# Performance work log

Measured on AMD Instinct MI355X. Metric: run time of the kernel, lower is better.

Reference implementation:

```python
import jax, jax.numpy as jnp
import numpy as np

T, DIM, HID = 8192, 1024, 4096

def setup_inputs() -> dict:
    key = jax.random.key(0)
    k1, k2, k3 = jax.random.split(key, 3)
    x = jax.random.normal(k1, (T, DIM), dtype=jnp.float32)
    # torch Linear weight layout: [out_features, in_features]
    W_fc = jax.random.normal(k2, (HID, DIM), dtype=jnp.float32) * 0.02
    W_proj = jax.random.normal(k3, (DIM, HID), dtype=jnp.float32) * 0.02
    return {"x": x, "W_fc": W_fc, "W_proj": W_proj}

def reference(x, W_fc, W_proj):
    # fc: x @ W_fc^T  -> relu -> square -> proj: @ W_proj^T
    h = jnp.einsum('td,hd->th', x, W_fc)      # [T, HID]
    h = jnp.square(jax.nn.relu(h))            # relu(h)^2 (relu^2 activation)
    return jnp.einsum('th,dh->td', h, W_proj) # [T, DIM]
```

## Files before the change

### kernel.cpp

```cpp
#include <hip/hip_runtime.h>
#include <stdint.h>


#define BM 128
#define BN 128
#define BK 64

typedef __attribute__((ext_vector_type(8))) short bf16x8;
typedef __attribute__((ext_vector_type(4))) float f32x4;

typedef const __attribute__((address_space(1))) unsigned int* gas_u32p;
typedef __attribute__((address_space(3))) unsigned int* las_u32p;

__device__ __forceinline__ void load16_to_lds(const void* gptr, void* lptr) {
    __builtin_amdgcn_global_load_lds((gas_u32p)gptr, (las_u32p)lptr, 16, 0, 0);
}

__device__ __forceinline__ unsigned short f2bf(float f) {
    unsigned int u = __float_as_uint(f);
    u += 0x7FFFu + ((u >> 16) & 1u);
    return (unsigned short)(u >> 16);
}

__global__ void cvt_all(const float4* __restrict__ x,  ushort4* __restrict__ xb,
                        const float4* __restrict__ wf, ushort4* __restrict__ wfb,
                        const float4* __restrict__ wp, ushort4* __restrict__ wpb)
{
    const int base = blockIdx.x * 1024 + threadIdx.x;
    #pragma unroll
    for (int j = 0; j < 4; j++) {
        const int i = base + j * 256;
        const float4* s; ushort4* d; int k;
        if (i < (1 << 21))            { s = x;  d = xb;  k = i; }
        else if (i < 3 * (1 << 20))   { s = wf; d = wfb; k = i - (1 << 21); }
        else                          { s = wp; d = wpb; k = i - 3 * (1 << 20); }
        float4 v = s[k];
        ushort4 o;
        o.x = f2bf(v.x); o.y = f2bf(v.y); o.z = f2bf(v.z); o.w = f2bf(v.w);
        d[k] = o;
    }
}

template<bool RELU2, bool OUT_BF16>
__global__ __launch_bounds__(256, 3)
void gemm_bt(const unsigned short* __restrict__ A,
             const unsigned short* __restrict__ B,
             void* __restrict__ Cv, int M, int N, int K)
{
    __shared__ unsigned short sA[BM * BK];
    __shared__ unsigned short sB[BN * BK];

    const int tid  = threadIdx.x;
    const int lane = tid & 63;
    const int wave = tid >> 6;
    const int wm   = (wave >> 1) * 64;
    const int wn   = (wave & 1) * 64;
    const int quad = lane >> 4;
    const int m16  = lane & 15;

    const long bm0 = (long)blockIdx.y * BM;
    const long bn0 = (long)blockIdx.x * BN;

    const int srow = tid >> 3;
    const int scol = (tid & 7) * 8;

    const unsigned short* gA = A + (bm0 + srow) * (long)K + scol;
    const unsigned short* gB = B + (bn0 + srow) * (long)K + scol;
    char* lA = (char*)sA + tid * 16;
    char* lB = (char*)sB + tid * 16;

    f32x4 acc[4][4];
    #pragma unroll
    for (int i = 0; i < 4; i++)
        #pragma unroll
        for (int j = 0; j < 4; j++)
            acc[i][j] = (f32x4)0.0f;

    for (int k0 = 0; k0 < K; k0 += BK) {
        #pragma unroll
        for (int c = 0; c < 4; c++)
            load16_to_lds(gA + (long)c * 32 * K + k0, lA + c * 4096);
        #pragma unroll
        for (int c = 0; c < 4; c++)
            load16_to_lds(gB + (long)c * 32 * K + k0, lB + c * 4096);
        __syncthreads();

        #pragma unroll
        for (int h = 0; h < 2; h++) {
            bf16x8 af[4], bfr[4];
            #pragma unroll
            for (int i = 0; i < 4; i++)
                af[i]  = *(const bf16x8*)&sA[(wm + i * 16 + m16) * BK + h * 32 + quad * 8];
            #pragma unroll
            for (int j = 0; j < 4; j++)
                bfr[j] = *(const bf16x8*)&sB[(wn + j * 16 + m16) * BK + h * 32 + quad * 8];

            #pragma unroll
            for (int i = 0; i < 4; i++)
                #pragma unroll
                for (int j = 0; j < 4; j++)
                    acc[i][j] = __builtin_amdgcn_mfma_f32_16x16x32_bf16(
                        af[i], bfr[j], acc[i][j], 0, 0, 0);
        }
        __syncthreads();
    }

    #pragma unroll
    for (int i = 0; i < 4; i++) {
        #pragma unroll
        for (int j = 0; j < 4; j++) {
            #pragma unroll
            for (int r = 0; r < 4; r++) {
                float v = acc[i][j][r];
                if (RELU2) v = (v > 0.0f) ? v * v : 0.0f;
                const long row = bm0 + wm + i * 16 + quad * 4 + r;
                const long col = bn0 + wn + j * 16 + m16;
                if (OUT_BF16)
                    ((unsigned short*)Cv)[row * (long)N + col] = f2bf(v);
                else
                    ((float*)Cv)[row * (long)N + col] = v;
            }
        }
    }
}

extern "C" void kernel_launch(void* const* d_in, const int* in_sizes, int n_in,
                              void* d_out, int out_size, void* d_ws, size_t ws_size,
                              hipStream_t stream) {
    (void)in_sizes; (void)n_in; (void)out_size; (void)ws_size;

    const int T = 8192, DIM = 1024, HID = 4096;

    const float* x     = (const float*)d_in[0];
    const float* W_fc  = (const float*)d_in[1];
    const float* W_prj = (const float*)d_in[2];
    float* out = (float*)d_out;

    char* ws = (char*)d_ws;
    unsigned short* h   = (unsigned short*)ws;
    unsigned short* xb  = (unsigned short*)(ws + (64l << 20));
    unsigned short* wfb = (unsigned short*)(ws + (80l << 20));
    unsigned short* wpb = (unsigned short*)(ws + (88l << 20));

    cvt_all<<<4096, 256, 0, stream>>>(
        (const float4*)x,     (ushort4*)xb,
        (const float4*)W_fc,  (ushort4*)wfb,
        (const float4*)W_prj, (ushort4*)wpb);

    gemm_bt<true, true><<<dim3(HID / BN, T / BM), dim3(256), 0, stream>>>(
        xb, wfb, h, T, HID, DIM);

    gemm_bt<false, false><<<dim3(DIM / BN, T / BM), dim3(256), 0, stream>>>(
        h, wpb, out, T, DIM, HID);
}
```

Measured before the change: 273.9 us.

## Replace GEMM with 8-wave 256-row tiled, double-buffered pipelined kernel

Replaces the 128x128 single-buffer GEMM with a 512-thread kernel that uses 256-row tiles and NF-dependent column tiles. It double-buffers LDS so the next k-slices are prefetched while MFMAs run, using interleaved barriers, explicit vmcnt waits and setprio. It also XOR-swizzles LDS offsets to avoid bank conflicts and remaps block IDs across 8 groups for cache locality. The cost is heavier register and LDS use per block, plus fragile hand-tuned wait counts.

```diff
diff --git a/kernel.cpp b/kernel.cpp
--- a/kernel.cpp
+++ b/kernel.cpp
@@ -1,10 +1,6 @@
 #include <hip/hip_runtime.h>
 #include <stdint.h>
 
-
-#define BM 128
-#define BN 128
-#define BK 64
 
 typedef __attribute__((ext_vector_type(8))) short bf16x8;
 typedef __attribute__((ext_vector_type(4))) float f32x4;
@@ -41,80 +37,179 @@
     }
 }
 
-template<bool RELU2, bool OUT_BF16>
-__global__ __launch_bounds__(256, 3)
-void gemm_bt(const unsigned short* __restrict__ A,
-             const unsigned short* __restrict__ B,
-             void* __restrict__ Cv, int M, int N, int K)
+#define LGKM0_FENCE() do { \
+    asm volatile("s_waitcnt lgkmcnt(0)" ::: "memory"); \
+    __builtin_amdgcn_sched_barrier(0); } while (0)
+
+template<int NF, bool RELU2, bool OUT_BF16>
+__global__ __launch_bounds__(512, 2)
+void gemm8p(const unsigned short* __restrict__ A,
+            const unsigned short* __restrict__ B,
+            void* __restrict__ Cv, int M, int N, int K)
 {
-    __shared__ unsigned short sA[BM * BK];
-    __shared__ unsigned short sB[BN * BK];
+    constexpr int BM   = 256;
+    constexpr int BN   = 64 * NF;
+    constexpr int CB   = BN / 128;
+    constexpr int AKH  = 16384;
+    constexpr int BKH  = BN * 64;
+    constexpr int BOFF = 2 * AKH;
+    constexpr int BUFB = 2 * AKH + 2 * BKH;
+    constexpr int KEEP = 2 + 2 * CB;
+    (void)M;
+
+    __shared__ char lds[2 * BUFB];
 
     const int tid  = threadIdx.x;
     const int lane = tid & 63;
     const int wave = tid >> 6;
-    const int wm   = (wave >> 1) * 64;
-    const int wn   = (wave & 1) * 64;
+    const int wm   = wave >> 2;
+    const int wn   = wave & 3;
     const int quad = lane >> 4;
     const int m16  = lane & 15;
 
-    const long bm0 = (long)blockIdx.y * BM;
-    const long bn0 = (long)blockIdx.x * BN;
-
-    const int srow = tid >> 3;
-    const int scol = (tid & 7) * 8;
-
-    const unsigned short* gA = A + (bm0 + srow) * (long)K + scol;
-    const unsigned short* gB = B + (bn0 + srow) * (long)K + scol;
-    char* lA = (char*)sA + tid * 16;
-    char* lB = (char*)sB + tid * 16;
-
-    f32x4 acc[4][4];
-    #pragma unroll
-    for (int i = 0; i < 4; i++)
-        #pragma unroll
-        for (int j = 0; j < 4; j++)
+    const int gx = gridDim.x;
+    int flat = blockIdx.y * gx + blockIdx.x;
+    const int cpx = (gx * gridDim.y) >> 3;
+    flat = (flat & 7) * cpx + (flat >> 3);
+    const long bm0 = (long)(flat / gx) * BM;
+    const long bn0 = (long)(flat % gx) * BN;
+
+    const int srow   = tid >> 2;
+    const int schunk = (tid & 3) ^ ((tid >> 3) & 3);
+    const unsigned short* gA = A + (bm0 + srow) * (long)K + schunk * 8;
+    const unsigned short* gB = B + (bn0 + srow) * (long)K + schunk * 8;
+    char* lbase = (char*)lds;
+
+    int offA[8], offB[NF];
+    #pragma unroll
+    for (int i = 0; i < 8; i++) {
+        const int lo = (wm * 128 + i * 16 + m16) * 64 + quad * 16;
+        offA[i] = lo ^ (((lo >> 7) & 3) << 4);
+    }
+    #pragma unroll
+    for (int j = 0; j < NF; j++) {
+        const int lo = (wn * 16 * NF + j * 16 + m16) * 64 + quad * 16;
+        offB[j] = lo ^ (((lo >> 7) & 3) << 4);
+    }
+
+    f32x4 acc[8][NF];
+    #pragma unroll
+    for (int i = 0; i < 8; i++)
+        #pragma unroll
+        for (int j = 0; j < NF; j++)
             acc[i][j] = (f32x4)0.0f;
 
-    for (int k0 = 0; k0 < K; k0 += BK) {
-        #pragma unroll
-        for (int c = 0; c < 4; c++)
-            load16_to_lds(gA + (long)c * 32 * K + k0, lA + c * 4096);
-        #pragma unroll
-        for (int c = 0; c < 4; c++)
-            load16_to_lds(gB + (long)c * 32 * K + k0, lB + c * 4096);
-        __syncthreads();
-
-        #pragma unroll
-        for (int h = 0; h < 2; h++) {
-            bf16x8 af[4], bfr[4];
-            #pragma unroll
-            for (int i = 0; i < 4; i++)
-                af[i]  = *(const bf16x8*)&sA[(wm + i * 16 + m16) * BK + h * 32 + quad * 8];
-            #pragma unroll
-            for (int j = 0; j < 4; j++)
-                bfr[j] = *(const bf16x8*)&sB[(wn + j * 16 + m16) * BK + h * 32 + quad * 8];
-
-            #pragma unroll
-            for (int i = 0; i < 4; i++)
-                #pragma unroll
-                for (int j = 0; j < 4; j++)
-                    acc[i][j] = __builtin_amdgcn_mfma_f32_16x16x32_bf16(
-                        af[i], bfr[j], acc[i][j], 0, 0, 0);
-        }
-        __syncthreads();
-    }
-
-    #pragma unroll
-    for (int i = 0; i < 4; i++) {
-        #pragma unroll
-        for (int j = 0; j < 4; j++) {
+    const int NT = K >> 6;
+
+    #define STAGE_A(t, kh) do { \
+        char* _d = lbase + ((t) & 1) * BUFB + (kh) * AKH + tid * 16; \
+        const unsigned short* _s = gA + (long)(t) * 64 + (kh) * 32; \
+        load16_to_lds(_s, _d); \
+        load16_to_lds(_s + 128l * K, _d + 8192); } while (0)
+
+    #define STAGE_B(t, kh) do { \
+        char* _d = lbase + ((t) & 1) * BUFB + BOFF + (kh) * BKH + tid * 16; \
+        const unsigned short* _s = gB + (long)(t) * 64 + (kh) * 32; \
+        load16_to_lds(_s, _d); \
+        if (CB == 2) load16_to_lds(_s + 128l * K, _d + 8192); } while (0)
+
+    STAGE_B(0, 0); STAGE_A(0, 0); STAGE_B(0, 1); STAGE_A(0, 1);
+    if (NT > 1) {
+        STAGE_B(1, 0); STAGE_A(1, 0); STAGE_B(1, 1);
+        asm volatile("s_waitcnt vmcnt(%0)" :: "i"(KEEP) : "memory");
+    } else {
+        asm volatile("s_waitcnt vmcnt(0)" ::: "memory");
+    }
+    __builtin_amdgcn_sched_barrier(0);
+    __builtin_amdgcn_s_barrier();
+
+    for (int t = 0; t < NT; ++t) {
+        char* bufA = lbase + (t & 1) * BUFB;
+        char* bufB = bufA + BOFF;
+        bf16x8 af[4], bf[NF];
+
+        #pragma unroll
+        for (int j = 0; j < NF; j++) bf[j] = *(const bf16x8*)(bufB + offB[j]);
+        #pragma unroll
+        for (int i = 0; i < 4; i++)  af[i] = *(const bf16x8*)(bufA + offA[i]);
+        if (t + 1 < NT) STAGE_A(t + 1, 1);
+        __builtin_amdgcn_s_barrier();
+        LGKM0_FENCE();
+        __builtin_amdgcn_s_setprio(1);
+        #pragma unroll
+        for (int i = 0; i < 4; i++)
+            #pragma unroll
+            for (int j = 0; j < NF; j++)
+                acc[i][j] = __builtin_amdgcn_mfma_f32_16x16x32_bf16(
+                    af[i], bf[j], acc[i][j], 0, 0, 0);
+        __builtin_amdgcn_s_setprio(0);
+        __builtin_amdgcn_s_barrier();
+
+        #pragma unroll
+        for (int i = 0; i < 4; i++)  af[i] = *(const bf16x8*)(bufA + offA[4 + i]);
+        if (t + 2 < NT) STAGE_B(t + 2, 0);
+        __builtin_amdgcn_s_barrier();
+        LGKM0_FENCE();
+        __builtin_amdgcn_s_setprio(1);
+        #pragma unroll
+        for (int i = 0; i < 4; i++)
+            #pragma unroll
+            for (int j = 0; j < NF; j++)
+                acc[4 + i][j] = __builtin_amdgcn_mfma_f32_16x16x32_bf16(
+                    af[i], bf[j], acc[4 + i][j], 0, 0, 0);
+        __builtin_amdgcn_s_setprio(0);
+        __builtin_amdgcn_s_barrier();
+
+        #pragma unroll
+        for (int j = 0; j < NF; j++) bf[j] = *(const bf16x8*)(bufB + BKH + offB[j]);
+        #pragma unroll
+        for (int i = 0; i < 4; i++)  af[i] = *(const bf16x8*)(bufA + AKH + offA[i]);
+        if (t + 2 < NT) STAGE_A(t + 2, 0);
+        __builtin_amdgcn_s_barrier();
+        LGKM0_FENCE();
+        __builtin_amdgcn_s_setprio(1);
+        #pragma unroll
+        for (int i = 0; i < 4; i++)
+            #pragma unroll
+            for (int j = 0; j < NF; j++)
+                acc[i][j] = __builtin_amdgcn_mfma_f32_16x16x32_bf16(
+                    af[i], bf[j], acc[i][j], 0, 0, 0);
+        __builtin_amdgcn_s_setprio(0);
+        __builtin_amdgcn_s_barrier();
+
+        #pragma unroll
+        for (int i = 0; i < 4; i++)  af[i] = *(const bf16x8*)(bufA + AKH + offA[4 + i]);
+        if (t + 2 < NT) STAGE_B(t + 2, 1);
+        __builtin_amdgcn_s_barrier();
+        LGKM0_FENCE();
+        __builtin_amdgcn_s_setprio(1);
+        #pragma unroll
+        for (int i = 0; i < 4; i++)
+            #pragma unroll
+            for (int j = 0; j < NF; j++)
+                acc[4 + i][j] = __builtin_amdgcn_mfma_f32_16x16x32_bf16(
+                    af[i], bf[j], acc[4 + i][j], 0, 0, 0);
+        __builtin_amdgcn_s_setprio(0);
+        if (t + 2 < NT) asm volatile("s_waitcnt vmcnt(%0)" :: "i"(KEEP) : "memory");
+        else            asm volatile("s_waitcnt vmcnt(0)" ::: "memory");
+        __builtin_amdgcn_sched_barrier(0);
+        __builtin_amdgcn_s_barrier();
+    }
+    #undef STAGE_A
+    #undef STAGE_B
+
+    const long baseRow = bm0 + wm * 128 + quad * 4;
+    const long baseCol = bn0 + wn * 16 * NF + m16;
+    #pragma unroll
+    for (int i = 0; i < 8; i++) {
+        #pragma unroll
+        for (int j = 0; j < NF; j++) {
             #pragma unroll
             for (int r = 0; r < 4; r++) {
                 float v = acc[i][j][r];
                 if (RELU2) v = (v > 0.0f) ? v * v : 0.0f;
-                const long row = bm0 + wm + i * 16 + quad * 4 + r;
-                const long col = bn0 + wn + j * 16 + m16;
+                const long row = baseRow + i * 16 + r;
+                const long col = baseCol + j * 16;
                 if (OUT_BF16)
                     ((unsigned short*)Cv)[row * (long)N + col] = f2bf(v);
                 else
@@ -147,9 +242,9 @@
         (const float4*)W_fc,  (ushort4*)wfb,
         (const float4*)W_prj, (ushort4*)wpb);
 
-    gemm_bt<true, true><<<dim3(HID / BN, T / BM), dim3(256), 0, stream>>>(
+    gemm8p<4, true, true><<<dim3(HID / 256, T / 256), dim3(512), 0, stream>>>(
         xb, wfb, h, T, HID, DIM);
 
-    gemm_bt<false, false><<<dim3(DIM / BN, T / BM), dim3(256), 0, stream>>>(
+    gemm8p<2, false, false><<<dim3(DIM / 128, T / 256), dim3(512), 0, stream>>>(
         h, wpb, out, T, DIM, HID);
 }
```

Measured after the change: 244.9 us. -10.6%, faster.
